# Performance work log

Measured on AMD Instinct MI355X. Metric: run time of the kernel, lower is better.

Reference implementation:

```python
import jax, jax.numpy as jnp
import numpy as np

GROUPS = 8
EPS = 1e-5


def setup_inputs() -> dict:
    key = jax.random.key(0)
    ks = jax.random.split(key, 7)
    b, c, h, w = 32, 256, 32, 32
    x = jax.random.normal(ks[0], (b, c, h, w), dtype=jnp.float32)
    gn_weight = jax.random.normal(ks[1], (c,), dtype=jnp.float32) * 0.02 + 1.0
    gn_bias = jax.random.normal(ks[2], (c,), dtype=jnp.float32) * 0.02
    w_qkv = jax.random.normal(ks[3], (3 * c, c), dtype=jnp.float32) / np.sqrt(c)
    b_qkv = jax.random.normal(ks[4], (3 * c,), dtype=jnp.float32) * 0.01
    w_out = jax.random.normal(ks[5], (c, c), dtype=jnp.float32) / np.sqrt(c)
    b_out = jax.random.normal(ks[6], (c,), dtype=jnp.float32) * 0.01
    return {"x": x, "gn_weight": gn_weight, "gn_bias": gn_bias,
            "w_qkv": w_qkv, "b_qkv": b_qkv, "w_out": w_out, "b_out": b_out}


def group_norm(x, weight, bias):
    b, c, h, w = x.shape
    xg = x.reshape(b, GROUPS, c // GROUPS, h, w)
    mean = jnp.mean(xg, axis=(2, 3, 4), keepdims=True)
    var = jnp.var(xg, axis=(2, 3, 4), keepdims=True)
    xg = (xg - mean) * jax.lax.rsqrt(var + EPS)
    x = xg.reshape(b, c, h, w)
    return x * weight[None, :, None, None] + bias[None, :, None, None]


def reference(x, gn_weight, gn_bias, w_qkv, b_qkv, w_out, b_out):
    b, c, h, w = x.shape
    x_norm = group_norm(x, gn_weight, gn_bias)
    # 1x1 conv == channel matmul: (b, 3c, h, w)
    qkv = jnp.einsum('oc,bchw->bohw', w_qkv, x_norm) + b_qkv[None, :, None, None]
    q, k, v = jnp.split(qkv, 3, axis=1)
    hw = h * w
    q = q.reshape(b, c, hw)  # used transposed: (b, hw, c)
    k = k.reshape(b, c, hw)
    v = v.reshape(b, c, hw)
    scale = 1.0 / jnp.sqrt(jnp.float32(c))
    attn = jax.nn.softmax(jnp.einsum('bcs,bct->bst', q, k) * scale, axis=-1)  # (b, hw, hw)
    out = jnp.einsum('bst,bct->bcs', attn, v).reshape(b, c, h, w)
    out = jnp.einsum('oc,bchw->bohw', w_out, out) + b_out[None, :, None, None]
    return out + x
```

## Files before the change

kernel.cpp:

```cpp
#include <hip/hip_runtime.h>
#include <hip/hip_bf16.h>


typedef __bf16 bf16x8 __attribute__((ext_vector_type(8)));
typedef __bf16 bf16x4 __attribute__((ext_vector_type(4)));
typedef float f32x4 __attribute__((ext_vector_type(4)));
typedef float f32x16 __attribute__((ext_vector_type(16)));

#define MFMA16(a, b, c) __builtin_amdgcn_mfma_f32_16x16x32_bf16(a, b, c, 0, 0, 0)
#define MFMA32(a, b, c) __builtin_amdgcn_mfma_f32_32x32x16_bf16(a, b, c, 0, 0, 0)

__global__ __launch_bounds__(256) void gn_kernel(const float* __restrict__ x,
                                                 const float* __restrict__ gw,
                                                 const float* __restrict__ gb,
                                                 __bf16* __restrict__ xnT) {
    __shared__ float red[8];
    __shared__ float stats[2];
    __shared__ __bf16 Lds[512][40];
    const int b = blockIdx.x >> 3, g = blockIdx.x & 7;
    const size_t base = ((size_t)b * 256 + g * 32) * 1024;
    const float* xp = x + base;
    const int t = threadIdx.x;

    float s = 0.f, s2 = 0.f;
    #pragma unroll
    for (int i = 0; i < 16; i++) {
        int j = i * 256 + t;
        float4 v0 = *(const float4*)(xp + (size_t)j * 8);
        float4 v1 = *(const float4*)(xp + (size_t)j * 8 + 4);
        s  += v0.x + v0.y + v0.z + v0.w + v1.x + v1.y + v1.z + v1.w;
        s2 += v0.x*v0.x + v0.y*v0.y + v0.z*v0.z + v0.w*v0.w
            + v1.x*v1.x + v1.y*v1.y + v1.z*v1.z + v1.w*v1.w;
    }
    #pragma unroll
    for (int o = 32; o > 0; o >>= 1) { s += __shfl_down(s, o, 64); s2 += __shfl_down(s2, o, 64); }
    const int wv = t >> 6;
    if ((t & 63) == 0) { red[wv * 2] = s; red[wv * 2 + 1] = s2; }
    __syncthreads();
    if (t == 0) {
        float ts = 0.f, ts2 = 0.f;
        for (int w = 0; w < 4; w++) { ts += red[w * 2]; ts2 += red[w * 2 + 1]; }
        float mean = ts / 32768.f;
        float var = ts2 / 32768.f - mean * mean;
        stats[0] = mean; stats[1] = rsqrtf(var + 1e-5f);
    }
    __syncthreads();
    const float mean = stats[0], inv = stats[1];

    const int c = t >> 3;
    const int so = (t & 7) * 4;
    const float ga = gw[g * 32 + c], be = gb[g * 32 + c];

    for (int chunk = 0; chunk < 1024; chunk += 512) {
        #pragma unroll
        for (int i = 0; i < 16; i++) {
            int sl = so + i * 32;
            float4 v = *(const float4*)(xp + (size_t)c * 1024 + chunk + sl);
            Lds[sl + 0][c] = (__bf16)((v.x - mean) * inv * ga + be);
            Lds[sl + 1][c] = (__bf16)((v.y - mean) * inv * ga + be);
            Lds[sl + 2][c] = (__bf16)((v.z - mean) * inv * ga + be);
            Lds[sl + 3][c] = (__bf16)((v.w - mean) * inv * ga + be);
        }
        __syncthreads();
        #pragma unroll
        for (int rr = 0; rr < 2; rr++) {
            int sl = rr * 256 + t;
            #pragma unroll
            for (int u = 0; u < 4; u++) {
                bf16x8 vv = *(const bf16x8*)&Lds[sl][u * 8];
                *(bf16x8*)&xnT[((size_t)b * 1024 + chunk + sl) * 256 + g * 32 + u * 8] = vv;
            }
        }
        __syncthreads();
    }
}

#define GEMM_TILE_BODY(W_, BmatRowBase_)                                            \
    f32x4 acc[4][4] = {};                                                           \
    for (int kk = 0; kk < 256; kk += 32) {                                          \
        {                                                                           \
            int r = t >> 1, kc = (t & 1) * 16;                                      \
            const float* wp = &W_[(size_t)(m0 + r) * 256 + kk + kc];                \
            float4 a0 = *(const float4*)wp;                                         \
            float4 a1 = *(const float4*)(wp + 4);                                   \
            float4 a2 = *(const float4*)(wp + 8);                                   \
            float4 a3 = *(const float4*)(wp + 12);                                  \
            bf16x8 av0, av1;                                                        \
            av0[0] = (__bf16)a0.x; av0[1] = (__bf16)a0.y; av0[2] = (__bf16)a0.z;    \
            av0[3] = (__bf16)a0.w; av0[4] = (__bf16)a1.x; av0[5] = (__bf16)a1.y;    \
            av0[6] = (__bf16)a1.z; av0[7] = (__bf16)a1.w;                           \
            av1[0] = (__bf16)a2.x; av1[1] = (__bf16)a2.y; av1[2] = (__bf16)a2.z;    \
            av1[3] = (__bf16)a2.w; av1[4] = (__bf16)a3.x; av1[5] = (__bf16)a3.y;    \
            av1[6] = (__bf16)a3.z; av1[7] = (__bf16)a3.w;                           \
            *(bf16x8*)&As[r][kc] = av0;                                             \
            *(bf16x8*)&As[r][kc + 8] = av1;                                         \
            const __bf16* bp = &(BmatRowBase_)[(size_t)(n0 + r) * 256 + kk + kc];   \
            *(bf16x8*)&Bs[r][kc] = *(const bf16x8*)bp;                              \
            *(bf16x8*)&Bs[r][kc + 8] = *(const bf16x8*)(bp + 8);                    \
        }                                                                           \
        __syncthreads();                                                            \
        bf16x8 af[4], bfv[4];                                                       \
        _Pragma("unroll")                                                           \
        for (int im = 0; im < 4; im++)                                              \
            af[im] = *(const bf16x8*)&As[wm + im * 16 + l16][quad * 8];             \
        _Pragma("unroll")                                                           \
        for (int in = 0; in < 4; in++)                                              \
            bfv[in] = *(const bf16x8*)&Bs[wn + in * 16 + l16][quad * 8];            \
        _Pragma("unroll")                                                           \
        for (int im = 0; im < 4; im++)                                              \
            _Pragma("unroll")                                                       \
            for (int in = 0; in < 4; in++)                                          \
                acc[im][in] = MFMA16(af[im], bfv[in], acc[im][in]);                 \
        __syncthreads();                                                            \
    }

__global__ __launch_bounds__(256) void qkv_gemm(const float* __restrict__ W,
                                                const float* __restrict__ bias,
                                                const __bf16* __restrict__ xnT,
                                                __bf16* __restrict__ qtr,
                                                __bf16* __restrict__ ktr,
                                                __bf16* __restrict__ vbuf) {
    __shared__ __bf16 As[128][40];
    __shared__ __bf16 Bs[128][40];
    const int b = blockIdx.z;
    const int n0 = blockIdx.x * 128, m0 = blockIdx.y * 128;
    const int t = threadIdx.x;
    const int wave = t >> 6, lane = t & 63, quad = lane >> 4, l16 = lane & 15;
    const int wm = (wave & 1) * 64, wn = (wave >> 1) * 64;
    const __bf16* brow = xnT + (size_t)b * 1024 * 256;

    GEMM_TILE_BODY(W, brow)

    #pragma unroll
    for (int im = 0; im < 4; im++) {
        #pragma unroll
        for (int in = 0; in < 4; in++) {
            int sg = n0 + wn + in * 16 + l16;
            int ob = m0 + wm + im * 16 + quad * 4;
            if (m0 < 512) {
                bf16x4 ov;
                #pragma unroll
                for (int r = 0; r < 4; r++) ov[r] = (__bf16)(acc[im][in][r] + bias[ob + r]);
                __bf16* dst = (m0 < 256) ? &qtr[((size_t)b * 1024 + sg) * 256 + ob]
                                         : &ktr[((size_t)b * 1024 + sg) * 256 + (ob - 256)];
                *(bf16x4*)dst = ov;
            } else {
                #pragma unroll
                for (int r = 0; r < 4; r++) {
                    float val = acc[im][in][r] + bias[ob + r];
                    vbuf[((size_t)b * 256 + (ob - 512 + r)) * 1024 + sg] = (__bf16)val;
                }
            }
        }
    }
}

__global__ __launch_bounds__(512, 2) void attn_kernel(const __bf16* __restrict__ qtr,
                                                      const __bf16* __restrict__ ktr,
                                                      const __bf16* __restrict__ vbuf,
                                                      __bf16* __restrict__ aoT) {
    __shared__ __bf16 Kt[2][32][260];
    __shared__ __bf16 Vs[2][256][36];
    __shared__ __bf16 Pl[4][32][72];
    __shared__ float Lred[4][2][32];
    const int b = blockIdx.x;
    const int tid = threadIdx.x;
    const int wave = tid >> 6, lane = tid & 63, half = lane >> 5, l31 = lane & 31;
    const int pair = wave & 3, th = wave >> 2;
    const int s0 = blockIdx.y * 128 + pair * 32;
    const float kscale = 0.09016844f;

    bf16x8 aq[16];
    #pragma unroll
    for (int ks = 0; ks < 16; ks++)
        aq[ks] = *(const bf16x8*)&qtr[((size_t)b * 1024 + s0 + l31) * 256 + ks * 16 + half * 8];

    const int k_row = tid >> 3;
    const int k_cb  = (tid & 7) * 8;
    const int v_c   = tid >> 1;
    const int v_th  = tid & 1;
    const size_t kbase = (size_t)b * 1024 * 256;
    const size_t vbase = (size_t)b * 256 * 1024;

    float l_part[16] = {};
    f32x16 o_acc[4] = {};

    for (int it = 0; it < 16; it++) {
        const int t0 = it * 64;
        #pragma unroll
        for (int u = 0; u < 4; u++) {
            bf16x8 kv = *(const bf16x8*)&ktr[kbase + (size_t)(t0 + k_row) * 256 + k_cb + u * 64];
            *(bf16x8*)&Kt[k_row >> 5][k_row & 31][k_cb + u * 64] = kv;
        }
        #pragma unroll
        for (int u = 0; u < 4; u++) {
            bf16x8 vv = *(const bf16x8*)&vbuf[vbase + (size_t)v_c * 1024 + t0 + v_th * 32 + u * 8];
            *(bf16x8*)&Vs[v_th][v_c][u * 8] = vv;
        }
        __syncthreads();

        f32x16 sc_a = {}, sc_b = {};
        #pragma unroll
        for (int ks = 0; ks < 8; ks++) {
            bf16x8 bk0 = *(const bf16x8*)&Kt[th][l31][ks * 16 + half * 8];
            bf16x8 bk1 = *(const bf16x8*)&Kt[th][l31][(ks + 8) * 16 + half * 8];
            sc_a = MFMA32(aq[ks], bk0, sc_a);
            sc_b = MFMA32(aq[ks + 8], bk1, sc_b);
        }
        #pragma unroll
        for (int r = 0; r < 16; r++) {
            float p = exp2f((sc_a[r] + sc_b[r]) * kscale);
            l_part[r] += p;
            int row = (r & 3) + 8 * (r >> 2) + 4 * half;
            Pl[pair][row][th * 32 + l31] = (__bf16)p;
        }
        __syncthreads();

        bf16x8 ap[4];
        #pragma unroll
        for (int kc = 0; kc < 4; kc++)
            ap[kc] = *(const bf16x8*)&Pl[pair][l31][kc * 16 + half * 8];
        #pragma unroll
        for (int n = 0; n < 4; n++) {
            int c = th * 128 + n * 32 + l31;
            #pragma unroll
            for (int kc = 0; kc < 4; kc++) {
                bf16x8 bv = *(const bf16x8*)&Vs[kc >> 1][c][(kc & 1) * 16 + half * 8];
                o_acc[n] = MFMA32(ap[kc], bv, o_acc[n]);
            }
        }
        __syncthreads();
    }

    float lsum[16];
    #pragma unroll
    for (int r = 0; r < 16; r++) {
        float l = l_part[r];
        #pragma unroll
        for (int m = 16; m > 0; m >>= 1) l += __shfl_xor(l, m, 32);
        lsum[r] = l;
        if (l31 == 0) {
            int row = (r & 3) + 8 * (r >> 2) + 4 * half;
            Lred[pair][th][row] = l;
        }
    }
    __syncthreads();
    #pragma unroll
    for (int r = 0; r < 16; r++) {
        int row = (r & 3) + 8 * (r >> 2) + 4 * half;
        float rinv = 1.0f / (lsum[r] + Lred[pair][1 - th][row]);
        #pragma unroll
        for (int n = 0; n < 4; n++) {
            int c = th * 128 + n * 32 + l31;
            aoT[((size_t)b * 1024 + s0 + row) * 256 + c] = (__bf16)(o_acc[n][r] * rinv);
        }
    }
}

__global__ __launch_bounds__(256) void proj_gemm(const float* __restrict__ W,
                                                 const float* __restrict__ bias,
                                                 const __bf16* __restrict__ aoT,
                                                 const float* __restrict__ resid,
                                                 float* __restrict__ Out) {
    __shared__ __bf16 As[128][40];
    __shared__ __bf16 Bs[128][40];
    const int b = blockIdx.z;
    const int n0 = blockIdx.x * 128, m0 = blockIdx.y * 128;
    const int t = threadIdx.x;
    const int wave = t >> 6, lane = t & 63, quad = lane >> 4, l16 = lane & 15;
    const int wm = (wave & 1) * 64, wn = (wave >> 1) * 64;
    const __bf16* brow = aoT + (size_t)b * 1024 * 256;

    GEMM_TILE_BODY(W, brow)

    #pragma unroll
    for (int im = 0; im < 4; im++) {
        #pragma unroll
        for (int in = 0; in < 4; in++) {
            int sg = n0 + wn + in * 16 + l16;
            int ob = m0 + wm + im * 16 + quad * 4;
            #pragma unroll
            for (int r = 0; r < 4; r++) {
                int o = ob + r;
                size_t idx = ((size_t)b * 256 + o) * 1024 + sg;
                Out[idx] = acc[im][in][r] + bias[o] + resid[idx];
            }
        }
    }
}

extern "C" void kernel_launch(void* const* d_in, const int* in_sizes, int n_in,
                              void* d_out, int out_size, void* d_ws, size_t ws_size,
                              hipStream_t stream) {
    const float* x    = (const float*)d_in[0];
    const float* gw   = (const float*)d_in[1];
    const float* gb   = (const float*)d_in[2];
    const float* wqkv = (const float*)d_in[3];
    const float* bqkv = (const float*)d_in[4];
    const float* wout = (const float*)d_in[5];
    const float* bout = (const float*)d_in[6];
    float* out = (float*)d_out;

    const size_t T16 = (size_t)32 * 1024 * 256;
    __bf16* xnT  = (__bf16*)d_ws;
    __bf16* qtr  = xnT + T16;
    __bf16* ktr  = qtr + T16;
    __bf16* vbuf = ktr + T16;
    __bf16* aoT  = vbuf + T16;

    gn_kernel<<<dim3(256), 256, 0, stream>>>(x, gw, gb, xnT);
    qkv_gemm<<<dim3(8, 6, 32), 256, 0, stream>>>(wqkv, bqkv, xnT, qtr, ktr, vbuf);
    attn_kernel<<<dim3(32, 8), 512, 0, stream>>>(qtr, ktr, vbuf, aoT);
    proj_gemm<<<dim3(8, 2, 32), 256, 0, stream>>>(wout, bout, aoT, x, out);
}
```

Baseline: 219.7 us.

## Preconvert weights to bf16 and prefetch double-width K tiles in GEMMs

Adds a small kernel that converts the QKV and output-projection weights to bf16 once per call, so the GEMMs no longer re-read and convert fp32 weights in every tile. The GEMM body now uses a K-step of 64 with register prefetch of the next tile while MFMAs run on the current one, halving the number of barrier pairs. The group-norm kernel moves to 512 threads with narrower per-thread loads. The cost is one extra kernel launch, an extra workspace buffer, and more LDS per GEMM block.

```diff
diff --git a/kernel.cpp b/kernel.cpp
--- a/kernel.cpp
+++ b/kernel.cpp
@@ -10,11 +10,24 @@
 #define MFMA16(a, b, c) __builtin_amdgcn_mfma_f32_16x16x32_bf16(a, b, c, 0, 0, 0)
 #define MFMA32(a, b, c) __builtin_amdgcn_mfma_f32_32x32x16_bf16(a, b, c, 0, 0, 0)
 
-__global__ __launch_bounds__(256) void gn_kernel(const float* __restrict__ x,
+__global__ __launch_bounds__(256) void wconv_kernel(const float* __restrict__ wqkv,
+                                                    const float* __restrict__ wout,
+                                                    __bf16* __restrict__ wbf) {
+    int idx = (blockIdx.x * 256 + threadIdx.x) * 8;
+    const float* src = (idx < 196608) ? (wqkv + idx) : (wout + (idx - 196608));
+    float4 v0 = *(const float4*)src;
+    float4 v1 = *(const float4*)(src + 4);
+    bf16x8 o;
+    o[0] = (__bf16)v0.x; o[1] = (__bf16)v0.y; o[2] = (__bf16)v0.z; o[3] = (__bf16)v0.w;
+    o[4] = (__bf16)v1.x; o[5] = (__bf16)v1.y; o[6] = (__bf16)v1.z; o[7] = (__bf16)v1.w;
+    *(bf16x8*)&wbf[idx] = o;
+}
+
+__global__ __launch_bounds__(512) void gn_kernel(const float* __restrict__ x,
                                                  const float* __restrict__ gw,
                                                  const float* __restrict__ gb,
                                                  __bf16* __restrict__ xnT) {
-    __shared__ float red[8];
+    __shared__ float red[16];
     __shared__ float stats[2];
     __shared__ __bf16 Lds[512][40];
     const int b = blockIdx.x >> 3, g = blockIdx.x & 7;
@@ -24,8 +37,8 @@
 
     float s = 0.f, s2 = 0.f;
     #pragma unroll
-    for (int i = 0; i < 16; i++) {
-        int j = i * 256 + t;
+    for (int i = 0; i < 8; i++) {
+        int j = i * 512 + t;
         float4 v0 = *(const float4*)(xp + (size_t)j * 8);
         float4 v1 = *(const float4*)(xp + (size_t)j * 8 + 4);
         s  += v0.x + v0.y + v0.z + v0.w + v1.x + v1.y + v1.z + v1.w;
@@ -39,7 +52,7 @@
     __syncthreads();
     if (t == 0) {
         float ts = 0.f, ts2 = 0.f;
-        for (int w = 0; w < 4; w++) { ts += red[w * 2]; ts2 += red[w * 2 + 1]; }
+        for (int w = 0; w < 8; w++) { ts += red[w * 2]; ts2 += red[w * 2 + 1]; }
         float mean = ts / 32768.f;
         float var = ts2 / 32768.f - mean * mean;
         stats[0] = mean; stats[1] = rsqrtf(var + 1e-5f);
@@ -47,24 +60,21 @@
     __syncthreads();
     const float mean = stats[0], inv = stats[1];
 
-    const int c = t >> 3;
-    const int so = (t & 7) * 4;
+    const int c = t >> 4;
+    const int so = (t & 15) * 2;
     const float ga = gw[g * 32 + c], be = gb[g * 32 + c];
 
     for (int chunk = 0; chunk < 1024; chunk += 512) {
         #pragma unroll
         for (int i = 0; i < 16; i++) {
             int sl = so + i * 32;
-            float4 v = *(const float4*)(xp + (size_t)c * 1024 + chunk + sl);
-            Lds[sl + 0][c] = (__bf16)((v.x - mean) * inv * ga + be);
+            float2 v = *(const float2*)(xp + (size_t)c * 1024 + chunk + sl);
+            Lds[sl][c]     = (__bf16)((v.x - mean) * inv * ga + be);
             Lds[sl + 1][c] = (__bf16)((v.y - mean) * inv * ga + be);
-            Lds[sl + 2][c] = (__bf16)((v.z - mean) * inv * ga + be);
-            Lds[sl + 3][c] = (__bf16)((v.w - mean) * inv * ga + be);
-        }
-        __syncthreads();
-        #pragma unroll
-        for (int rr = 0; rr < 2; rr++) {
-            int sl = rr * 256 + t;
+        }
+        __syncthreads();
+        {
+            int sl = t;
             #pragma unroll
             for (int u = 0; u < 4; u++) {
                 bf16x8 vv = *(const bf16x8*)&Lds[sl][u * 8];
@@ -75,61 +85,64 @@
     }
 }
 
-#define GEMM_TILE_BODY(W_, BmatRowBase_)                                            \
-    f32x4 acc[4][4] = {};                                                           \
-    for (int kk = 0; kk < 256; kk += 32) {                                          \
-        {                                                                           \
-            int r = t >> 1, kc = (t & 1) * 16;                                      \
-            const float* wp = &W_[(size_t)(m0 + r) * 256 + kk + kc];                \
-            float4 a0 = *(const float4*)wp;                                         \
-            float4 a1 = *(const float4*)(wp + 4);                                   \
-            float4 a2 = *(const float4*)(wp + 8);                                   \
-            float4 a3 = *(const float4*)(wp + 12);                                  \
-            bf16x8 av0, av1;                                                        \
-            av0[0] = (__bf16)a0.x; av0[1] = (__bf16)a0.y; av0[2] = (__bf16)a0.z;    \
-            av0[3] = (__bf16)a0.w; av0[4] = (__bf16)a1.x; av0[5] = (__bf16)a1.y;    \
-            av0[6] = (__bf16)a1.z; av0[7] = (__bf16)a1.w;                           \
-            av1[0] = (__bf16)a2.x; av1[1] = (__bf16)a2.y; av1[2] = (__bf16)a2.z;    \
-            av1[3] = (__bf16)a2.w; av1[4] = (__bf16)a3.x; av1[5] = (__bf16)a3.y;    \
-            av1[6] = (__bf16)a3.z; av1[7] = (__bf16)a3.w;                           \
-            *(bf16x8*)&As[r][kc] = av0;                                             \
-            *(bf16x8*)&As[r][kc + 8] = av1;                                         \
-            const __bf16* bp = &(BmatRowBase_)[(size_t)(n0 + r) * 256 + kk + kc];   \
-            *(bf16x8*)&Bs[r][kc] = *(const bf16x8*)bp;                              \
-            *(bf16x8*)&Bs[r][kc + 8] = *(const bf16x8*)(bp + 8);                    \
-        }                                                                           \
-        __syncthreads();                                                            \
-        bf16x8 af[4], bfv[4];                                                       \
-        _Pragma("unroll")                                                           \
-        for (int im = 0; im < 4; im++)                                              \
-            af[im] = *(const bf16x8*)&As[wm + im * 16 + l16][quad * 8];             \
-        _Pragma("unroll")                                                           \
-        for (int in = 0; in < 4; in++)                                              \
-            bfv[in] = *(const bf16x8*)&Bs[wn + in * 16 + l16][quad * 8];            \
-        _Pragma("unroll")                                                           \
-        for (int im = 0; im < 4; im++)                                              \
-            _Pragma("unroll")                                                       \
-            for (int in = 0; in < 4; in++)                                          \
-                acc[im][in] = MFMA16(af[im], bfv[in], acc[im][in]);                 \
-        __syncthreads();                                                            \
-    }
-
-__global__ __launch_bounds__(256) void qkv_gemm(const float* __restrict__ W,
+#define GEMM64_BODY(ArowBase_, BrowBase_)                                               \
+    f32x4 acc[4][4] = {};                                                               \
+    const int r_ = t >> 1, kc_ = (t & 1) * 32;                                          \
+    bf16x8 pa[4], pb[4];                                                                \
+    _Pragma("unroll")                                                                   \
+    for (int u = 0; u < 4; u++) {                                                       \
+        pa[u] = *(const bf16x8*)&(ArowBase_)[(size_t)r_ * 256 + kc_ + u * 8];           \
+        pb[u] = *(const bf16x8*)&(BrowBase_)[(size_t)r_ * 256 + kc_ + u * 8];           \
+    }                                                                                   \
+    for (int kk = 0; kk < 256; kk += 64) {                                              \
+        _Pragma("unroll")                                                               \
+        for (int u = 0; u < 4; u++) {                                                   \
+            *(bf16x8*)&As[r_][kc_ + u * 8] = pa[u];                                     \
+            *(bf16x8*)&Bs[r_][kc_ + u * 8] = pb[u];                                     \
+        }                                                                               \
+        __syncthreads();                                                                \
+        if (kk < 192) {                                                                 \
+            _Pragma("unroll")                                                           \
+            for (int u = 0; u < 4; u++) {                                               \
+                pa[u] = *(const bf16x8*)&(ArowBase_)[(size_t)r_ * 256 + kk + 64 + kc_ + u * 8]; \
+                pb[u] = *(const bf16x8*)&(BrowBase_)[(size_t)r_ * 256 + kk + 64 + kc_ + u * 8]; \
+            }                                                                           \
+        }                                                                               \
+        _Pragma("unroll")                                                               \
+        for (int kh = 0; kh < 2; kh++) {                                                \
+            bf16x8 af[4], bfv[4];                                                       \
+            _Pragma("unroll")                                                           \
+            for (int im = 0; im < 4; im++)                                              \
+                af[im] = *(const bf16x8*)&As[wm + im * 16 + l16][kh * 32 + quad * 8];   \
+            _Pragma("unroll")                                                           \
+            for (int in = 0; in < 4; in++)                                              \
+                bfv[in] = *(const bf16x8*)&Bs[wn + in * 16 + l16][kh * 32 + quad * 8];  \
+            _Pragma("unroll")                                                           \
+            for (int im = 0; im < 4; im++)                                              \
+                _Pragma("unroll")                                                       \
+                for (int in = 0; in < 4; in++)                                          \
+                    acc[im][in] = MFMA16(af[im], bfv[in], acc[im][in]);                 \
+        }                                                                               \
+        __syncthreads();                                                                \
+    }
+
+__global__ __launch_bounds__(256) void qkv_gemm(const __bf16* __restrict__ wbf,
                                                 const float* __restrict__ bias,
                                                 const __bf16* __restrict__ xnT,
                                                 __bf16* __restrict__ qtr,
                                                 __bf16* __restrict__ ktr,
                                                 __bf16* __restrict__ vbuf) {
-    __shared__ __bf16 As[128][40];
-    __shared__ __bf16 Bs[128][40];
+    __shared__ __bf16 As[128][72];
+    __shared__ __bf16 Bs[128][72];
     const int b = blockIdx.z;
     const int n0 = blockIdx.x * 128, m0 = blockIdx.y * 128;
     const int t = threadIdx.x;
     const int wave = t >> 6, lane = t & 63, quad = lane >> 4, l16 = lane & 15;
     const int wm = (wave & 1) * 64, wn = (wave >> 1) * 64;
-    const __bf16* brow = xnT + (size_t)b * 1024 * 256;
-
-    GEMM_TILE_BODY(W, brow)
+    const __bf16* arow = wbf + (size_t)m0 * 256;
+    const __bf16* brow = xnT + ((size_t)b * 1024 + n0) * 256;
+
+    GEMM64_BODY(arow, brow)
 
     #pragma unroll
     for (int im = 0; im < 4; im++) {
@@ -257,21 +270,22 @@
     }
 }
 
-__global__ __launch_bounds__(256) void proj_gemm(const float* __restrict__ W,
+__global__ __launch_bounds__(256) void proj_gemm(const __bf16* __restrict__ wbf_out,
                                                  const float* __restrict__ bias,
                                                  const __bf16* __restrict__ aoT,
                                                  const float* __restrict__ resid,
                                                  float* __restrict__ Out) {
-    __shared__ __bf16 As[128][40];
-    __shared__ __bf16 Bs[128][40];
+    __shared__ __bf16 As[128][72];
+    __shared__ __bf16 Bs[128][72];
     const int b = blockIdx.z;
     const int n0 = blockIdx.x * 128, m0 = blockIdx.y * 128;
     const int t = threadIdx.x;
     const int wave = t >> 6, lane = t & 63, quad = lane >> 4, l16 = lane & 15;
     const int wm = (wave & 1) * 64, wn = (wave >> 1) * 64;
-    const __bf16* brow = aoT + (size_t)b * 1024 * 256;
-
-    GEMM_TILE_BODY(W, brow)
+    const __bf16* arow = wbf_out + (size_t)m0 * 256;
+    const __bf16* brow = aoT + ((size_t)b * 1024 + n0) * 256;
+
+    GEMM64_BODY(arow, brow)
 
     #pragma unroll
     for (int im = 0; im < 4; im++) {
@@ -307,9 +321,11 @@
     __bf16* ktr  = qtr + T16;
     __bf16* vbuf = ktr + T16;
     __bf16* aoT  = vbuf + T16;
-
-    gn_kernel<<<dim3(256), 256, 0, stream>>>(x, gw, gb, xnT);
-    qkv_gemm<<<dim3(8, 6, 32), 256, 0, stream>>>(wqkv, bqkv, xnT, qtr, ktr, vbuf);
+    __bf16* wbf  = aoT + T16;
+
+    wconv_kernel<<<dim3(128), 256, 0, stream>>>(wqkv, wout, wbf);
+    gn_kernel<<<dim3(256), 512, 0, stream>>>(x, gw, gb, xnT);
+    qkv_gemm<<<dim3(8, 6, 32), 256, 0, stream>>>(wbf, bqkv, xnT, qtr, ktr, vbuf);
     attn_kernel<<<dim3(32, 8), 512, 0, stream>>>(qtr, ktr, vbuf, aoT);
-    proj_gemm<<<dim3(8, 2, 32), 256, 0, stream>>>(wout, bout, aoT, x, out);
-}
+    proj_gemm<<<dim3(8, 2, 32), 256, 0, stream>>>(wbf + 196608, bout, aoT, x, out);
+}
```

New measurement: 211.4 us. 1.04x faster.
